# Performance work log

Hardware: AMD Instinct MI355X
Metric: run time of the kernel (lower is better)

## Reference

```python
import jax, jax.numpy as jnp
import numpy as np

N_HEADS = 16
D_MODEL = 1024
D_HEAD = D_MODEL // N_HEADS  # 64


def setup_inputs() -> dict:
    key = jax.random.key(0)
    ks = jax.random.split(key, 7)
    B, S = 16, 1024
    x = jax.random.normal(ks[0], (B, S, D_MODEL), dtype=jnp.float32)
    # Per-head torch Linear params: weight [out, in] = [D_HEAD, D_HEAD], bias [D_HEAD].
    # Xavier-uniform scale for square weight: sqrt(6/(fan_in+fan_out)).
    lim = float(np.sqrt(6.0 / (D_HEAD + D_HEAD)))
    blim = float(1.0 / np.sqrt(D_HEAD))  # torch default bias init U(-1/sqrt(fan_in), ...)
    Wq = jax.random.uniform(ks[1], (N_HEADS, D_HEAD, D_HEAD), jnp.float32, -lim, lim)
    Wk = jax.random.uniform(ks[2], (N_HEADS, D_HEAD, D_HEAD), jnp.float32, -lim, lim)
    Wv = jax.random.uniform(ks[3], (N_HEADS, D_HEAD, D_HEAD), jnp.float32, -lim, lim)
    bq = jax.random.uniform(ks[4], (N_HEADS, D_HEAD), jnp.float32, -blim, blim)
    bk = jax.random.uniform(ks[5], (N_HEADS, D_HEAD), jnp.float32, -blim, blim)
    bv = jax.random.uniform(ks[6], (N_HEADS, D_HEAD), jnp.float32, -blim, blim)
    return {"sequences": x, "Wq": Wq, "Wk": Wk, "Wv": Wv, "bq": bq, "bk": bk, "bv": bv}


def reference(sequences, Wq, Wk, Wv, bq, bk, bv):
    B, S, D = sequences.shape
    H, dh = N_HEADS, D_HEAD
    # Split feature dim into heads: [B, S, H, dh] (same chunks the torch loop slices).
    x = sequences.reshape(B, S, H, dh)
    # torch Linear: y = x @ W.T + b  -> einsum over the 'in' axis of W[out, in].
    q = jnp.einsum("bshd,hed->bshe", x, Wq) + bq  # [B,S,H,dh]
    k = jnp.einsum("bshd,hed->bshe", x, Wk) + bk
    v = jnp.einsum("bshd,hed->bshe", x, Wv) + bv
    scale = 1.0 / jnp.sqrt(jnp.asarray(dh, dtype=sequences.dtype))
    scores = jnp.einsum("bshe,bthe->bhst", q, k) * scale  # [B,H,S,S]
    weights = jax.nn.softmax(scores, axis=-1)
    attended = jnp.einsum("bhst,bthe->bshe", weights, v)  # [B,S,H,dh]
    # hstack over heads == concat along feature dim.
    return attended.reshape(B, S, D)
```

## Files before the change

kernel.cpp:

```cpp
#include <hip/hip_runtime.h>

constexpr int B_ = 16, S_ = 1024, H_ = 16, DH_ = 64, DM_ = 1024;

typedef short bf16x8 __attribute__((ext_vector_type(8)));
typedef unsigned short us8 __attribute__((ext_vector_type(8)));
typedef unsigned short us4 __attribute__((ext_vector_type(4)));
typedef float f32x4 __attribute__((ext_vector_type(4)));
typedef float f32x16 __attribute__((ext_vector_type(16)));
typedef unsigned u32x4 __attribute__((ext_vector_type(4)));

__device__ __forceinline__ unsigned short f2b(float f) {
    unsigned u = __builtin_bit_cast(unsigned, f);
    u += 0x7FFFu + ((u >> 16) & 1u);
    return (unsigned short)(u >> 16);
}

__device__ __forceinline__ int swz(int r, int c) { return (r << 6) + (c ^ ((r & 7) << 3)); }

__device__ __forceinline__ unsigned cvtpk(float lo, float hi) {
    unsigned r;
    asm("v_cvt_pk_bf16_f32 %0, %1, %2" : "=v"(r) : "v"(lo), "v"(hi));
    return r;
}
__device__ __forceinline__ void permswap(unsigned& a, unsigned& b) {
    asm volatile("v_permlane32_swap_b32 %0, %1" : "+v"(a), "+v"(b));
}

#define QSCALE 0.18033688011112042f

__global__ __launch_bounds__(256) void proj_kernel(
    const float* __restrict__ x,
    const float* __restrict__ wq, const float* __restrict__ wk, const float* __restrict__ wv,
    const float* __restrict__ bq, const float* __restrict__ bk, const float* __restrict__ bv,
    unsigned short* __restrict__ qo, unsigned short* __restrict__ ko,
    unsigned short* __restrict__ vto)
{
    __shared__ unsigned short xs[128 * 64];
    __shared__ unsigned short wls[3][64 * 64];

    const int tid = threadIdx.x;
    const int bid = blockIdx.x;
    const int chunk = bid & 7, bh = bid >> 3;
    const int b = bh >> 4, h = bh & 15;
    const int s0 = chunk * 128;
    const int lane = tid & 63, w = tid >> 6;
    const int lr = lane & 15, lg = lane >> 4;

    #pragma unroll
    for (int it = 0; it < 4; ++it) {
        int item = it * 256 + tid;
        int row = item >> 3, c = (item & 7) << 3;
        const float* src = x + (size_t)(b * S_ + s0 + row) * DM_ + h * DH_ + c;
        float4 f0 = *(const float4*)src;
        float4 f1 = *(const float4*)(src + 4);
        us8 v = { f2b(f0.x), f2b(f0.y), f2b(f0.z), f2b(f0.w),
                  f2b(f1.x), f2b(f1.y), f2b(f1.z), f2b(f1.w) };
        *(us8*)&xs[swz(row, c)] = v;
    }
    const float* wsrc[3] = { wq, wk, wv };
    #pragma unroll
    for (int mtx = 0; mtx < 3; ++mtx) {
        const float scl = (mtx == 0) ? QSCALE : 1.0f;
        #pragma unroll
        for (int it = 0; it < 2; ++it) {
            int item = it * 256 + tid;
            int row = item >> 3, c = (item & 7) << 3;
            const float* src = wsrc[mtx] + (size_t)h * 4096 + row * 64 + c;
            float4 f0 = *(const float4*)src;
            float4 f1 = *(const float4*)(src + 4);
            us8 v = { f2b(f0.x * scl), f2b(f0.y * scl), f2b(f0.z * scl), f2b(f0.w * scl),
                      f2b(f1.x * scl), f2b(f1.y * scl), f2b(f1.z * scl), f2b(f1.w * scl) };
            *(us8*)&wls[mtx][swz(row, c)] = v;
        }
    }
    __syncthreads();

    bf16x8 af[2][2];
    #pragma unroll
    for (int mt = 0; mt < 2; ++mt)
        #pragma unroll
        for (int k2 = 0; k2 < 2; ++k2)
            af[mt][k2] = *(const bf16x8*)&xs[swz(w * 32 + mt * 16 + lr, k2 * 32 + lg * 8)];

    const float* bias[3] = { bq, bk, bv };
    #pragma unroll
    for (int mtx = 0; mtx < 3; ++mtx) {
        const float bscl = (mtx == 0) ? QSCALE : 1.0f;
        #pragma unroll
        for (int mt = 0; mt < 2; ++mt) {
            #pragma unroll
            for (int n4 = 0; n4 < 4; ++n4) {
                f32x4 acc = { 0.f, 0.f, 0.f, 0.f };
                #pragma unroll
                for (int k2 = 0; k2 < 2; ++k2) {
                    bf16x8 bf_ = *(const bf16x8*)&wls[mtx][swz(n4 * 16 + lr, k2 * 32 + lg * 8)];
                    acc = __builtin_amdgcn_mfma_f32_16x16x32_bf16(af[mt][k2], bf_, acc, 0, 0, 0);
                }
                const int e = n4 * 16 + lr;
                const float bb = bias[mtx][h * DH_ + e] * bscl;
                const int srow0 = s0 + w * 32 + mt * 16 + lg * 4;
                if (mtx == 0) {
                    #pragma unroll
                    for (int r = 0; r < 4; ++r)
                        qo[(size_t)(bh * S_ + srow0 + r) * 64 + e] = f2b(acc[r] + bb);
                } else if (mtx == 1) {
                    #pragma unroll
                    for (int r = 0; r < 4; ++r)
                        ko[(size_t)(bh * S_ + srow0 + r) * 64 + e] = f2b(acc[r] + bb);
                } else {
                    us4 pk = { f2b(acc[0] + bb), f2b(acc[1] + bb),
                               f2b(acc[2] + bb), f2b(acc[3] + bb) };
                    *(us4*)&vto[(size_t)(bh * 64 + e) * S_ + srow0] = pk;
                }
            }
        }
    }
}

__global__ __launch_bounds__(256) void attn_kernel(
    const unsigned short* __restrict__ qw, const unsigned short* __restrict__ kw,
    const unsigned short* __restrict__ vtw, float* __restrict__ out)
{
    __shared__ unsigned short ks[2][64 * 64];
    __shared__ unsigned short vs[2][64 * 64];

    const int tid = threadIdx.x, lane = tid & 63, w = tid >> 6;
    int bid = blockIdx.x;
    bid = (bid & 7) * 256 + (bid >> 3);
    const int qt = bid & 7, bh = bid >> 3;
    const int b = bh >> 4, h = bh & 15;
    const int q0 = qt * 128;
    const int l31 = lane & 31, hi = lane >> 5, hi8 = hi << 3;

    const unsigned short* kbase = kw + (size_t)bh * S_ * 64;
    const unsigned short* vbase = vtw + (size_t)bh * 64 * S_;

    bf16x8 qf[4];
    {
        const unsigned short* qp = qw + (size_t)(bh * S_ + q0 + w * 32 + l31) * 64 + hi8;
        #pragma unroll
        for (int s = 0; s < 4; ++s) qf[s] = *(const bf16x8*)(qp + s * 16);
    }

    const int srow = tid >> 3, sc = (tid & 7) << 3;
    const int swzA = swz(srow, sc), swzB = swz(srow + 32, sc);

    const short ONE = (short)0x3F80;
    const bf16x8 ones = { ONE, ONE, ONE, ONE, ONE, ONE, ONE, ONE };

    f32x16 o0, o1, lsum, zro;
    #pragma unroll
    for (int i = 0; i < 16; ++i) { o0[i] = 0.f; o1[i] = 0.f; lsum[i] = 0.f; zro[i] = 0.f; }

    us8 sk0 = *(const us8*)(kbase + (size_t)srow * 64 + sc);
    us8 sk1 = *(const us8*)(kbase + (size_t)(srow + 32) * 64 + sc);
    us8 sv0 = *(const us8*)(vbase + (size_t)srow * S_ + sc);
    us8 sv1 = *(const us8*)(vbase + (size_t)(srow + 32) * S_ + sc);
    *(us8*)&ks[0][swzA] = sk0;  *(us8*)&ks[0][swzB] = sk1;
    *(us8*)&vs[0][swzA] = sv0;  *(us8*)&vs[0][swzB] = sv1;
    __syncthreads();

    constexpr int NT = S_ / 64;
    for (int t = 0; t < NT; ++t) {
        const int cur = t & 1;

        if (t + 1 < NT) {
            const int n1 = (t + 1) * 64;
            sk0 = *(const us8*)(kbase + (size_t)(n1 + srow) * 64 + sc);
            sk1 = *(const us8*)(kbase + (size_t)(n1 + srow + 32) * 64 + sc);
            sv0 = *(const us8*)(vbase + (size_t)srow * S_ + n1 + sc);
            sv1 = *(const us8*)(vbase + (size_t)(srow + 32) * S_ + n1 + sc);
        }

        f32x16 p0, p1;
        {
            bf16x8 ka0 = *(const bf16x8*)&ks[cur][swz(l31,      hi8)];
            bf16x8 ka1 = *(const bf16x8*)&ks[cur][swz(32 + l31, hi8)];
            p0 = __builtin_amdgcn_mfma_f32_32x32x16_bf16(ka0, qf[0], zro, 0, 0, 0);
            p1 = __builtin_amdgcn_mfma_f32_32x32x16_bf16(ka1, qf[0], zro, 0, 0, 0);
        }
        #pragma unroll
        for (int s = 1; s < 4; ++s) {
            bf16x8 ka0 = *(const bf16x8*)&ks[cur][swz(l31,      s * 16 + hi8)];
            bf16x8 ka1 = *(const bf16x8*)&ks[cur][swz(32 + l31, s * 16 + hi8)];
            p0 = __builtin_amdgcn_mfma_f32_32x32x16_bf16(ka0, qf[s], p0, 0, 0, 0);
            p1 = __builtin_amdgcn_mfma_f32_32x32x16_bf16(ka1, qf[s], p1, 0, 0, 0);
        }

        #pragma unroll
        for (int i = 0; i < 16; ++i) {
            p0[i] = __builtin_amdgcn_exp2f(p0[i]);
            p1[i] = __builtin_amdgcn_exp2f(p1[i]);
        }

        bf16x8 pa[4];
        {
            unsigned a0 = cvtpk(p0[0], p0[1]),  b0 = cvtpk(p0[4], p0[5]);
            unsigned a1 = cvtpk(p0[2], p0[3]),  b1 = cvtpk(p0[6], p0[7]);
            permswap(a0, b0); permswap(a1, b1);
            u32x4 t0 = { a0, a1, b0, b1 };
            pa[0] = __builtin_bit_cast(bf16x8, t0);
            unsigned a2 = cvtpk(p0[8], p0[9]),   b2 = cvtpk(p0[12], p0[13]);
            unsigned a3 = cvtpk(p0[10], p0[11]), b3 = cvtpk(p0[14], p0[15]);
            permswap(a2, b2); permswap(a3, b3);
            u32x4 t1 = { a2, a3, b2, b3 };
            pa[1] = __builtin_bit_cast(bf16x8, t1);
            unsigned a4 = cvtpk(p1[0], p1[1]),  b4 = cvtpk(p1[4], p1[5]);
            unsigned a5 = cvtpk(p1[2], p1[3]),  b5 = cvtpk(p1[6], p1[7]);
            permswap(a4, b4); permswap(a5, b5);
            u32x4 t2 = { a4, a5, b4, b5 };
            pa[2] = __builtin_bit_cast(bf16x8, t2);
            unsigned a6 = cvtpk(p1[8], p1[9]),   b6 = cvtpk(p1[12], p1[13]);
            unsigned a7 = cvtpk(p1[10], p1[11]), b7 = cvtpk(p1[14], p1[15]);
            permswap(a6, b6); permswap(a7, b7);
            u32x4 t3 = { a6, a7, b6, b7 };
            pa[3] = __builtin_bit_cast(bf16x8, t3);
        }

        #pragma unroll
        for (int s = 0; s < 4; ++s) {
            bf16x8 vb0 = *(const bf16x8*)&vs[cur][swz(l31,      s * 16 + hi8)];
            bf16x8 vb1 = *(const bf16x8*)&vs[cur][swz(32 + l31, s * 16 + hi8)];
            o0 = __builtin_amdgcn_mfma_f32_32x32x16_bf16(pa[s], vb0, o0, 0, 0, 0);
            o1 = __builtin_amdgcn_mfma_f32_32x32x16_bf16(pa[s], vb1, o1, 0, 0, 0);
            lsum = __builtin_amdgcn_mfma_f32_32x32x16_bf16(pa[s], ones, lsum, 0, 0, 0);
        }

        if (t + 1 < NT) {
            const int nb = cur ^ 1;
            *(us8*)&ks[nb][swzA] = sk0;  *(us8*)&ks[nb][swzB] = sk1;
            *(us8*)&vs[nb][swzA] = sv0;  *(us8*)&vs[nb][swzB] = sv1;
        }
        __syncthreads();
    }

    #pragma unroll
    for (int r = 0; r < 16; ++r) {
        const int q = (r & 3) + 8 * (r >> 2) + (hi << 2);
        const float iv = 1.0f / lsum[r];
        float* op = out + (size_t)(b * S_ + q0 + w * 32 + q) * DM_ + h * DH_ + l31;
        op[0]  = o0[r] * iv;
        op[32] = o1[r] * iv;
    }
}

extern "C" void kernel_launch(void* const* d_in, const int* in_sizes, int n_in,
                              void* d_out, int out_size, void* d_ws, size_t ws_size,
                              hipStream_t stream) {
    const float* x  = (const float*)d_in[0];
    const float* wq = (const float*)d_in[1];
    const float* wk = (const float*)d_in[2];
    const float* wv = (const float*)d_in[3];
    const float* bq = (const float*)d_in[4];
    const float* bk = (const float*)d_in[5];
    const float* bv = (const float*)d_in[6];
    float* out = (float*)d_out;

    const size_t per = (size_t)B_ * H_ * S_ * DH_;
    unsigned short* qws  = (unsigned short*)d_ws;
    unsigned short* kws  = qws + per;
    unsigned short* vtws = kws + per;

    proj_kernel<<<dim3(2048), dim3(256), 0, stream>>>(x, wq, wk, wv, bq, bk, bv,
                                                      qws, kws, vtws);
    attn_kernel<<<dim3(2048), dim3(256), 0, stream>>>(qws, kws, vtws, out);
}
```

Baseline: 134.6 us.

## Pipeline attention loop with direct-to-LDS loads, triple buffering and QK/PV overlap

Replaces the register-staged K/V copies with global_load_lds 16-byte loads written straight into LDS. The XOR swizzle moves to the global column index so the LDS layout matches the existing swz reader. K/V buffers grow from two to three, and the loop is software-pipelined so the QK^T MFMAs for tile t+1 are issued together with the exp/PV work for tile t. The aim is to hide load latency and keep the MFMA units busy, at the cost of more LDS, more live registers, and reliance on the barrier's implicit wait for the direct-to-LDS loads.

```diff
diff --git a/kernel.cpp b/kernel.cpp
--- a/kernel.cpp
+++ b/kernel.cpp
@@ -24,6 +24,12 @@
 }
 __device__ __forceinline__ void permswap(unsigned& a, unsigned& b) {
     asm volatile("v_permlane32_swap_b32 %0, %1" : "+v"(a), "+v"(b));
+}
+
+__device__ __forceinline__ void gload16(const unsigned short* g, unsigned short* l) {
+    __builtin_amdgcn_global_load_lds(
+        (const __attribute__((address_space(1))) void*)g,
+        (__attribute__((address_space(3))) void*)l, 16, 0, 0);
 }
 
 #define QSCALE 0.18033688011112042f
@@ -117,12 +123,73 @@
     }
 }
 
+__device__ __forceinline__ void qk_tile(const unsigned short* K, const bf16x8 (&qf)[4],
+                                        const f32x16& zro, f32x16& p0, f32x16& p1,
+                                        int l31, int hi8)
+{
+    {
+        bf16x8 ka0 = *(const bf16x8*)&K[swz(l31,      hi8)];
+        bf16x8 ka1 = *(const bf16x8*)&K[swz(32 + l31, hi8)];
+        p0 = __builtin_amdgcn_mfma_f32_32x32x16_bf16(ka0, qf[0], zro, 0, 0, 0);
+        p1 = __builtin_amdgcn_mfma_f32_32x32x16_bf16(ka1, qf[0], zro, 0, 0, 0);
+    }
+    #pragma unroll
+    for (int s = 1; s < 4; ++s) {
+        bf16x8 ka0 = *(const bf16x8*)&K[swz(l31,      s * 16 + hi8)];
+        bf16x8 ka1 = *(const bf16x8*)&K[swz(32 + l31, s * 16 + hi8)];
+        p0 = __builtin_amdgcn_mfma_f32_32x32x16_bf16(ka0, qf[s], p0, 0, 0, 0);
+        p1 = __builtin_amdgcn_mfma_f32_32x32x16_bf16(ka1, qf[s], p1, 0, 0, 0);
+    }
+}
+
+__device__ __forceinline__ void pv_tile(f32x16& p0, f32x16& p1, const unsigned short* V,
+                                        const bf16x8& ones, f32x16& o0, f32x16& o1,
+                                        f32x16& lsum, int l31, int hi8)
+{
+    #pragma unroll
+    for (int i = 0; i < 16; ++i) {
+        p0[i] = __builtin_amdgcn_exp2f(p0[i]);
+        p1[i] = __builtin_amdgcn_exp2f(p1[i]);
+    }
+    bf16x8 pa[4];
+    {
+        unsigned a0 = cvtpk(p0[0], p0[1]),  b0 = cvtpk(p0[4], p0[5]);
+        unsigned a1 = cvtpk(p0[2], p0[3]),  b1 = cvtpk(p0[6], p0[7]);
+        permswap(a0, b0); permswap(a1, b1);
+        u32x4 t0 = { a0, a1, b0, b1 };
+        pa[0] = __builtin_bit_cast(bf16x8, t0);
+        unsigned a2 = cvtpk(p0[8], p0[9]),   b2 = cvtpk(p0[12], p0[13]);
+        unsigned a3 = cvtpk(p0[10], p0[11]), b3 = cvtpk(p0[14], p0[15]);
+        permswap(a2, b2); permswap(a3, b3);
+        u32x4 t1 = { a2, a3, b2, b3 };
+        pa[1] = __builtin_bit_cast(bf16x8, t1);
+        unsigned a4 = cvtpk(p1[0], p1[1]),  b4 = cvtpk(p1[4], p1[5]);
+        unsigned a5 = cvtpk(p1[2], p1[3]),  b5 = cvtpk(p1[6], p1[7]);
+        permswap(a4, b4); permswap(a5, b5);
+        u32x4 t2 = { a4, a5, b4, b5 };
+        pa[2] = __builtin_bit_cast(bf16x8, t2);
+        unsigned a6 = cvtpk(p1[8], p1[9]),   b6 = cvtpk(p1[12], p1[13]);
+        unsigned a7 = cvtpk(p1[10], p1[11]), b7 = cvtpk(p1[14], p1[15]);
+        permswap(a6, b6); permswap(a7, b7);
+        u32x4 t3 = { a6, a7, b6, b7 };
+        pa[3] = __builtin_bit_cast(bf16x8, t3);
+    }
+    #pragma unroll
+    for (int s = 0; s < 4; ++s) {
+        bf16x8 vb0 = *(const bf16x8*)&V[swz(l31,      s * 16 + hi8)];
+        bf16x8 vb1 = *(const bf16x8*)&V[swz(32 + l31, s * 16 + hi8)];
+        o0 = __builtin_amdgcn_mfma_f32_32x32x16_bf16(pa[s], vb0, o0, 0, 0, 0);
+        o1 = __builtin_amdgcn_mfma_f32_32x32x16_bf16(pa[s], vb1, o1, 0, 0, 0);
+        lsum = __builtin_amdgcn_mfma_f32_32x32x16_bf16(pa[s], ones, lsum, 0, 0, 0);
+    }
+}
+
 __global__ __launch_bounds__(256) void attn_kernel(
     const unsigned short* __restrict__ qw, const unsigned short* __restrict__ kw,
     const unsigned short* __restrict__ vtw, float* __restrict__ out)
 {
-    __shared__ unsigned short ks[2][64 * 64];
-    __shared__ unsigned short vs[2][64 * 64];
+    __shared__ unsigned short ks[3][64 * 64];
+    __shared__ unsigned short vs[3][64 * 64];
 
     const int tid = threadIdx.x, lane = tid & 63, w = tid >> 6;
     int bid = blockIdx.x;
@@ -135,6 +202,19 @@
     const unsigned short* kbase = kw + (size_t)bh * S_ * 64;
     const unsigned short* vbase = vtw + (size_t)bh * 64 * S_;
 
+    const int srow8 = lane >> 3;
+    const int colsw = ((lane & 7) ^ (lane >> 3)) << 3;
+
+    auto stage = [&](int t, int bf) {
+        const int n1 = t * 64;
+        #pragma unroll
+        for (int i = 0; i < 2; ++i) {
+            const int br = i * 32 + (w << 3);
+            gload16(kbase + (size_t)(n1 + br + srow8) * 64 + colsw, &ks[bf][br * 64]);
+            gload16(vbase + (size_t)(br + srow8) * S_ + n1 + colsw, &vs[bf][br * 64]);
+        }
+    };
+
     bf16x8 qf[4];
     {
         const unsigned short* qp = qw + (size_t)(bh * S_ + q0 + w * 32 + l31) * 64 + hi8;
@@ -142,9 +222,6 @@
         for (int s = 0; s < 4; ++s) qf[s] = *(const bf16x8*)(qp + s * 16);
     }
 
-    const int srow = tid >> 3, sc = (tid & 7) << 3;
-    const int swzA = swz(srow, sc), swzB = swz(srow + 32, sc);
-
     const short ONE = (short)0x3F80;
     const bf16x8 ones = { ONE, ONE, ONE, ONE, ONE, ONE, ONE, ONE };
 
@@ -152,87 +229,35 @@
     #pragma unroll
     for (int i = 0; i < 16; ++i) { o0[i] = 0.f; o1[i] = 0.f; lsum[i] = 0.f; zro[i] = 0.f; }
 
-    us8 sk0 = *(const us8*)(kbase + (size_t)srow * 64 + sc);
-    us8 sk1 = *(const us8*)(kbase + (size_t)(srow + 32) * 64 + sc);
-    us8 sv0 = *(const us8*)(vbase + (size_t)srow * S_ + sc);
-    us8 sv1 = *(const us8*)(vbase + (size_t)(srow + 32) * S_ + sc);
-    *(us8*)&ks[0][swzA] = sk0;  *(us8*)&ks[0][swzB] = sk1;
-    *(us8*)&vs[0][swzA] = sv0;  *(us8*)&vs[0][swzB] = sv1;
+    stage(0, 0);
+    stage(1, 1);
     __syncthreads();
 
+    f32x16 pA0, pA1, pB0, pB1;
+    qk_tile(&ks[0][0], qf, zro, pA0, pA1, l31, hi8);
+
     constexpr int NT = S_ / 64;
-    for (int t = 0; t < NT; ++t) {
-        const int cur = t & 1;
-
-        if (t + 1 < NT) {
-            const int n1 = (t + 1) * 64;
-            sk0 = *(const us8*)(kbase + (size_t)(n1 + srow) * 64 + sc);
-            sk1 = *(const us8*)(kbase + (size_t)(n1 + srow + 32) * 64 + sc);
-            sv0 = *(const us8*)(vbase + (size_t)srow * S_ + n1 + sc);
-            sv1 = *(const us8*)(vbase + (size_t)(srow + 32) * S_ + n1 + sc);
-        }
-
-        f32x16 p0, p1;
-        {
-            bf16x8 ka0 = *(const bf16x8*)&ks[cur][swz(l31,      hi8)];
-            bf16x8 ka1 = *(const bf16x8*)&ks[cur][swz(32 + l31, hi8)];
-            p0 = __builtin_amdgcn_mfma_f32_32x32x16_bf16(ka0, qf[0], zro, 0, 0, 0);
-            p1 = __builtin_amdgcn_mfma_f32_32x32x16_bf16(ka1, qf[0], zro, 0, 0, 0);
-        }
-        #pragma unroll
-        for (int s = 1; s < 4; ++s) {
-            bf16x8 ka0 = *(const bf16x8*)&ks[cur][swz(l31,      s * 16 + hi8)];
-            bf16x8 ka1 = *(const bf16x8*)&ks[cur][swz(32 + l31, s * 16 + hi8)];
-            p0 = __builtin_amdgcn_mfma_f32_32x32x16_bf16(ka0, qf[s], p0, 0, 0, 0);
-            p1 = __builtin_amdgcn_mfma_f32_32x32x16_bf16(ka1, qf[s], p1, 0, 0, 0);
-        }
-
-        #pragma unroll
-        for (int i = 0; i < 16; ++i) {
-            p0[i] = __builtin_amdgcn_exp2f(p0[i]);
-            p1[i] = __builtin_amdgcn_exp2f(p1[i]);
-        }
-
-        bf16x8 pa[4];
-        {
-            unsigned a0 = cvtpk(p0[0], p0[1]),  b0 = cvtpk(p0[4], p0[5]);
-            unsigned a1 = cvtpk(p0[2], p0[3]),  b1 = cvtpk(p0[6], p0[7]);
-            permswap(a0, b0); permswap(a1, b1);
-            u32x4 t0 = { a0, a1, b0, b1 };
-            pa[0] = __builtin_bit_cast(bf16x8, t0);
-            unsigned a2 = cvtpk(p0[8], p0[9]),   b2 = cvtpk(p0[12], p0[13]);
-            unsigned a3 = cvtpk(p0[10], p0[11]), b3 = cvtpk(p0[14], p0[15]);
-            permswap(a2, b2); permswap(a3, b3);
-            u32x4 t1 = { a2, a3, b2, b3 };
-            pa[1] = __builtin_bit_cast(bf16x8, t1);
-            unsigned a4 = cvtpk(p1[0], p1[1]),  b4 = cvtpk(p1[4], p1[5]);
-            unsigned a5 = cvtpk(p1[2], p1[3]),  b5 = cvtpk(p1[6], p1[7]);
-            permswap(a4, b4); permswap(a5, b5);
-            u32x4 t2 = { a4, a5, b4, b5 };
-            pa[2] = __builtin_bit_cast(bf16x8, t2);
-            unsigned a6 = cvtpk(p1[8], p1[9]),   b6 = cvtpk(p1[12], p1[13]);
-            unsigned a7 = cvtpk(p1[10], p1[11]), b7 = cvtpk(p1[14], p1[15]);
-            permswap(a6, b6); permswap(a7, b7);
-            u32x4 t3 = { a6, a7, b6, b7 };
-            pa[3] = __builtin_bit_cast(bf16x8, t3);
-        }
-
-        #pragma unroll
-        for (int s = 0; s < 4; ++s) {
-            bf16x8 vb0 = *(const bf16x8*)&vs[cur][swz(l31,      s * 16 + hi8)];
-            bf16x8 vb1 = *(const bf16x8*)&vs[cur][swz(32 + l31, s * 16 + hi8)];
-            o0 = __builtin_amdgcn_mfma_f32_32x32x16_bf16(pa[s], vb0, o0, 0, 0, 0);
-            o1 = __builtin_amdgcn_mfma_f32_32x32x16_bf16(pa[s], vb1, o1, 0, 0, 0);
-            lsum = __builtin_amdgcn_mfma_f32_32x32x16_bf16(pa[s], ones, lsum, 0, 0, 0);
-        }
-
-        if (t + 1 < NT) {
-            const int nb = cur ^ 1;
-            *(us8*)&ks[nb][swzA] = sk0;  *(us8*)&ks[nb][swzB] = sk1;
-            *(us8*)&vs[nb][swzA] = sv0;  *(us8*)&vs[nb][swzB] = sv1;
-        }
+    int bT = 0, bT1 = 1, bT2 = 2;
+    int t = 0;
+
+    #pragma unroll 1
+    for (int tt = 0; tt < 7; ++tt) {
         __syncthreads();
-    }
+        if (t + 2 < NT) stage(t + 2, bT2);
+        qk_tile(&ks[bT1][0], qf, zro, pB0, pB1, l31, hi8);
+        pv_tile(pA0, pA1, &vs[bT][0], ones, o0, o1, lsum, l31, hi8);
+        { int x = bT; bT = bT1; bT1 = bT2; bT2 = x; } ++t;
+        __syncthreads();
+        if (t + 2 < NT) stage(t + 2, bT2);
+        qk_tile(&ks[bT1][0], qf, zro, pA0, pA1, l31, hi8);
+        pv_tile(pB0, pB1, &vs[bT][0], ones, o0, o1, lsum, l31, hi8);
+        { int x = bT; bT = bT1; bT1 = bT2; bT2 = x; } ++t;
+    }
+    __syncthreads();
+    qk_tile(&ks[bT1][0], qf, zro, pB0, pB1, l31, hi8);
+    pv_tile(pA0, pA1, &vs[bT][0], ones, o0, o1, lsum, l31, hi8);
+    { int x = bT; bT = bT1; bT1 = bT2; bT2 = x; }
+    pv_tile(pB0, pB1, &vs[bT][0], ones, o0, o1, lsum, l31, hi8);
 
     #pragma unroll
     for (int r = 0; r < 16; ++r) {
```

After: 130.2 us. 1.03x faster.
